# Kernel tuning notes

Hardware: AMD Instinct MI355X
Metric: run time of the kernel (lower is better)

The kernel has to match this reference:

```python
import jax, jax.numpy as jnp
import numpy as np

# Plane-stress elasticity constants (E=1.0, nu=0.3), matching ModelXToResult.__init__
E_MOD = 1.0
NU = 0.3
C11 = E_MOD / (1.0 - NU ** 2)          # = c22
C12 = E_MOD * NU / (1.0 - NU ** 2)     # = c21
C33 = E_MOD / (2.0 * (1.0 + NU))

HIDDEN = 256


def setup_inputs() -> dict:
    key = jax.random.key(0)
    ks = jax.random.split(key, 5)
    B, N = 4, 65536
    X = jax.random.uniform(ks[0], (B, N, 2), dtype=jnp.float32)
    # MLP params (2 -> 256 -> 256 -> 256 -> 2), scaled ~ 1/sqrt(fan_in)
    W1 = jax.random.normal(ks[1], (2, HIDDEN), dtype=jnp.float32) / np.sqrt(2.0)
    b1 = jnp.zeros((HIDDEN,), jnp.float32)
    W2 = jax.random.normal(ks[2], (HIDDEN, HIDDEN), dtype=jnp.float32) / np.sqrt(HIDDEN)
    b2 = jnp.zeros((HIDDEN,), jnp.float32)
    W3 = jax.random.normal(ks[3], (HIDDEN, HIDDEN), dtype=jnp.float32) / np.sqrt(HIDDEN)
    b3 = jnp.zeros((HIDDEN,), jnp.float32)
    Wo = jax.random.normal(ks[4], (HIDDEN, 2), dtype=jnp.float32) / np.sqrt(HIDDEN)
    bo = jnp.zeros((2,), jnp.float32)
    return {"X": X, "W1": W1, "b1": b1, "W2": W2, "b2": b2,
            "W3": W3, "b3": b3, "Wo": Wo, "bo": bo}


def _disp(xy, W1, b1, W2, b2, W3, b3, Wo, bo):
    # xy: [B, N, 2] -> displacement [B, N, 2] = (u, v)
    h = jnp.tanh(xy @ W1 + b1)
    h = jnp.tanh(h @ W2 + b2)
    h = jnp.tanh(h @ W3 + b3)
    return h @ Wo + bo


def reference(X, W1, b1, W2, b2, W3, b3, Wo, bo):
    f = lambda xy: _disp(xy, W1, b1, W2, b2, W3, b3, Wo, bo)
    ones = jnp.ones_like(X[..., 0:1])
    zeros = jnp.zeros_like(ones)
    tx = jnp.concatenate([ones, zeros], axis=-1)  # d/dx tangent
    ty = jnp.concatenate([zeros, ones], axis=-1)  # d/dy tangent
    # Fused forward + full 2x2 Jacobian via two forward-mode JVPs
    out, d_dx = jax.jvp(f, (X,), (tx,))
    _, d_dy = jax.jvp(f, (X,), (ty,))
    u, v = out[..., 0:1], out[..., 1:2]
    u_x, v_x = d_dx[..., 0:1], d_dx[..., 1:2]
    u_y, v_y = d_dy[..., 0:1], d_dy[..., 1:2]
    u_xy = u_y + v_x
    stress_x = C11 * u_x + C12 * v_y
    stress_y = C12 * u_x + C11 * v_y
    stress_xy = C33 * u_xy
    strain_energy_density = 0.5 * (stress_x * u_x + stress_y * v_y + stress_xy * u_xy)
    return (u, v, stress_x, stress_y, stress_xy, strain_energy_density)
```

## Files before the change

### kernel.cpp

```cpp
#include <hip/hip_runtime.h>

#define HIDDEN 256
#define NPTS (4*65536)
#define MTILE 32
#define NWG (NPTS/MTILE)
#define THREADS 512

typedef _Float16 h8  __attribute__((ext_vector_type(8)));
typedef float    f4  __attribute__((ext_vector_type(4)));

__device__ __forceinline__ float tanh_fast(float x){
  float t = exp2f(x * 2.885390081777927f);
  return 1.0f - 2.0f * __builtin_amdgcn_rcpf(t + 1.0f);
}

__device__ __forceinline__ uint2 pack4(float a, float b, float c, float d){
  uint2 r;
  r.x = __builtin_bit_cast(unsigned int, __builtin_amdgcn_cvt_pkrtz(a, b));
  r.y = __builtin_bit_cast(unsigned int, __builtin_amdgcn_cvt_pkrtz(c, d));
  return r;
}

__device__ __forceinline__ int act_off(int p, int ubyte){
  return p*512 + (ubyte ^ ((p & 15) << 4));
}

__global__ void pack_weights(const float* __restrict__ W, _Float16* __restrict__ dst){
  int i = blockIdx.x * blockDim.x + threadIdx.x;
  int l  = i & 63;
  int nt = (i >> 6) & 15;
  int ks = i >> 10;
  int k0 = ks*32 + ((l >> 4) << 3);
  int n  = nt*16 + (l & 15);
  h8 v;
  #pragma unroll
  for (int j = 0; j < 8; ++j) v[j] = (_Float16)W[(k0 + j)*HIDDEN + n];
  *reinterpret_cast<h8*>(dst + (size_t)i*8) = v;
}

__launch_bounds__(THREADS, 4)
__global__ void pinn_fused(const float* __restrict__ X,
                           const float* __restrict__ W1,
                           const float* __restrict__ b1,
                           const float* __restrict__ b2,
                           const float* __restrict__ b3,
                           const float* __restrict__ Wo,
                           const float* __restrict__ bo,
                           const _Float16* __restrict__ Wp,
                           float* __restrict__ out)
{
  __shared__ __align__(16) char actS[3*MTILE*512];

  const int tid = threadIdx.x;
  const int wid = tid >> 6;
  const int l   = tid & 63;
  const int lg  = l >> 4;
  const int lr  = l & 15;
  const int Uq  = wid >> 1;
  const int Pg  = wid & 1;

  {
    const int pl = tid >> 4;
    const int ug = tid & 15;
    const int P  = blockIdx.x * MTILE + pl;
    const float x0 = X[2*P + 0];
    const float x1 = X[2*P + 1];
    #pragma unroll
    for (int c = 0; c < 4; ++c){
      const int u = ug*16 + c*4;
      const f4 w0 = *reinterpret_cast<const f4*>(W1 + u);
      const f4 w1 = *reinterpret_cast<const f4*>(W1 + HIDDEN + u);
      const f4 bb = *reinterpret_cast<const f4*>(b1 + u);
      float h[4], gx[4], gy[4];
      #pragma unroll
      for (int j = 0; j < 4; ++j){
        const float z = x0*w0[j] + x1*w1[j] + bb[j];
        const float t = tanh_fast(z);
        const float s = 1.0f - t*t;
        h[j]  = t;
        gx[j] = s * w0[j];
        gy[j] = s * w1[j];
      }
      const int off = act_off(pl, u*2);
      *reinterpret_cast<uint2*>(actS + 0*16384 + off) = pack4(h[0],h[1],h[2],h[3]);
      *reinterpret_cast<uint2*>(actS + 1*16384 + off) = pack4(gx[0],gx[1],gx[2],gx[3]);
      *reinterpret_cast<uint2*>(actS + 2*16384 + off) = pack4(gy[0],gy[1],gy[2],gy[3]);
    }
  }
  __syncthreads();

  for (int layer = 0; layer < 2; ++layer){
    const _Float16* WL = Wp + layer*65536;
    const float* bl = (layer == 0) ? b2 : b3;

    f4 acc[3][4];
    const f4 fzero = {0.f, 0.f, 0.f, 0.f};
    #pragma unroll
    for (int s = 0; s < 3; ++s)
      #pragma unroll
      for (int ut = 0; ut < 4; ++ut)
        acc[s][ut] = fzero;

    #pragma unroll
    for (int ks = 0; ks < 8; ++ks){
      h8 wf[4];
      #pragma unroll
      for (int ut = 0; ut < 4; ++ut)
        wf[ut] = *reinterpret_cast<const h8*>(WL + ((size_t)((ks*16 + Uq*4 + ut)*64 + l))*8);
      const int p   = Pg*16 + lr;
      const int ub  = ks*64 + lg*16;
      const int off = act_off(p, ub);
      #pragma unroll
      for (int s = 0; s < 3; ++s){
        const h8 af = *reinterpret_cast<const h8*>(actS + s*16384 + off);
        #pragma unroll
        for (int ut = 0; ut < 4; ++ut)
          acc[s][ut] = __builtin_amdgcn_mfma_f32_16x16x32_f16(wf[ut], af, acc[s][ut], 0, 0, 0);
      }
    }
    __syncthreads();

    #pragma unroll
    for (int ut = 0; ut < 4; ++ut){
      const int u0 = Uq*64 + ut*16 + lg*4;
      const f4 bb = *reinterpret_cast<const f4*>(bl + u0);
      const int p  = Pg*16 + lr;
      const f4 z  = acc[0][ut];
      const f4 zx = acc[1][ut];
      const f4 zy = acc[2][ut];
      float h[4], gx[4], gy[4];
      #pragma unroll
      for (int j = 0; j < 4; ++j){
        const float t = tanh_fast(z[j] + bb[j]);
        const float s = 1.0f - t*t;
        h[j]  = t;
        gx[j] = s * zx[j];
        gy[j] = s * zy[j];
      }
      const int off = act_off(p, u0*2);
      *reinterpret_cast<uint2*>(actS + 0*16384 + off) = pack4(h[0],h[1],h[2],h[3]);
      *reinterpret_cast<uint2*>(actS + 1*16384 + off) = pack4(gx[0],gx[1],gx[2],gx[3]);
      *reinterpret_cast<uint2*>(actS + 2*16384 + off) = pack4(gy[0],gy[1],gy[2],gy[3]);
    }
    __syncthreads();
  }

  {
    const int pl = tid >> 4;
    const int kg = tid & 15;
    const int P  = blockIdx.x * MTILE + pl;
    float au=0.f, av=0.f, aux=0.f, avx=0.f, auy=0.f, avy=0.f;
    #pragma unroll
    for (int c = 0; c < 2; ++c){
      const int k0  = kg*16 + c*8;
      const int off = act_off(pl, k0*2);
      const h8 hh = *reinterpret_cast<const h8*>(actS + 0*16384 + off);
      const h8 hx = *reinterpret_cast<const h8*>(actS + 1*16384 + off);
      const h8 hy = *reinterpret_cast<const h8*>(actS + 2*16384 + off);
      #pragma unroll
      for (int j = 0; j < 8; ++j){
        const float2 wo = *reinterpret_cast<const float2*>(Wo + 2*(k0 + j));
        const float fh = (float)hh[j];
        const float fx = (float)hx[j];
        const float fy = (float)hy[j];
        au  += fh*wo.x;  av  += fh*wo.y;
        aux += fx*wo.x;  avx += fx*wo.y;
        auy += fy*wo.x;  avy += fy*wo.y;
      }
    }
    #pragma unroll
    for (int m = 1; m < 16; m <<= 1){
      au  += __shfl_xor(au,  m, 64);
      av  += __shfl_xor(av,  m, 64);
      aux += __shfl_xor(aux, m, 64);
      avx += __shfl_xor(avx, m, 64);
      auy += __shfl_xor(auy, m, 64);
      avy += __shfl_xor(avy, m, 64);
    }
    if (kg == 0){
      const float C11 = 1.0989010989010988f;
      const float C12 = 0.32967032967032966f;
      const float C33 = 0.38461538461538464f;
      const float u  = au + bo[0];
      const float v  = av + bo[1];
      const float ux = aux, vx = avx, uy = auy, vy = avy;
      const float uxy = uy + vx;
      const float sx  = C11*ux + C12*vy;
      const float sy  = C12*ux + C11*vy;
      const float sxy = C33*uxy;
      const float sed = 0.5f*(sx*ux + sy*vy + sxy*uxy);
      out[0*NPTS + P] = u;
      out[1*NPTS + P] = v;
      out[2*NPTS + P] = sx;
      out[3*NPTS + P] = sy;
      out[4*NPTS + P] = sxy;
      out[5*NPTS + P] = sed;
    }
  }
}

extern "C" void kernel_launch(void* const* d_in, const int* in_sizes, int n_in,
                              void* d_out, int out_size, void* d_ws, size_t ws_size,
                              hipStream_t stream)
{
  const float* X  = (const float*)d_in[0];
  const float* W1 = (const float*)d_in[1];
  const float* b1 = (const float*)d_in[2];
  const float* W2 = (const float*)d_in[3];
  const float* b2 = (const float*)d_in[4];
  const float* W3 = (const float*)d_in[5];
  const float* b3 = (const float*)d_in[6];
  const float* Wo = (const float*)d_in[7];
  const float* bo = (const float*)d_in[8];

  _Float16* Wp = (_Float16*)d_ws;

  pack_weights<<<32, 256, 0, stream>>>(W2, Wp);
  pack_weights<<<32, 256, 0, stream>>>(W3, Wp + 65536);
  pinn_fused<<<NWG, THREADS, 0, stream>>>(X, W1, b1, b2, b3, Wo, bo, Wp, (float*)d_out);
}
```

Before: 290.8 us.

## Halve tile to 16 points and fuse output layer into last MFMA epilogue

Shrinks each workgroup to 16 points and 4 waves (256 threads), raising the occupancy hint from 4 to 6, and unrolls the two hidden layers explicitly. The last hidden layer's tanh and its JVP tangents are now reduced directly against Wo in registers instead of being written back to LDS and reread. Partial sums are reduced with cross-lane shuffles and a small LDS buffer shared across waves. This removes one LDS round trip and one barrier per tile. In exchange, each workgroup loads the same packed weights for half as many points, which doubles weight traffic from L2 per point.

```diff
diff --git a/kernel.cpp b/kernel.cpp
--- a/kernel.cpp
+++ b/kernel.cpp
@@ -2,9 +2,9 @@
 
 #define HIDDEN 256
 #define NPTS (4*65536)
-#define MTILE 32
+#define MTILE 16
 #define NWG (NPTS/MTILE)
-#define THREADS 512
+#define THREADS 256
 
 typedef _Float16 h8  __attribute__((ext_vector_type(8)));
 typedef float    f4  __attribute__((ext_vector_type(4)));
@@ -38,7 +38,7 @@
   *reinterpret_cast<h8*>(dst + (size_t)i*8) = v;
 }
 
-__launch_bounds__(THREADS, 4)
+__launch_bounds__(THREADS, 6)
 __global__ void pinn_fused(const float* __restrict__ X,
                            const float* __restrict__ W1,
                            const float* __restrict__ b1,
@@ -50,21 +50,19 @@
                            float* __restrict__ out)
 {
   __shared__ __align__(16) char actS[3*MTILE*512];
+  __shared__ __align__(16) float partS[MTILE*24];
 
   const int tid = threadIdx.x;
-  const int wid = tid >> 6;
   const int l   = tid & 63;
   const int lg  = l >> 4;
   const int lr  = l & 15;
-  const int Uq  = wid >> 1;
-  const int Pg  = wid & 1;
+  const int Uq  = __builtin_amdgcn_readfirstlane(tid >> 6);
 
   {
-    const int pl = tid >> 4;
-    const int ug = tid & 15;
+    const int pl = tid & 15;
+    const int ug = tid >> 4;
     const int P  = blockIdx.x * MTILE + pl;
-    const float x0 = X[2*P + 0];
-    const float x1 = X[2*P + 1];
+    const float2 xy = *reinterpret_cast<const float2*>(X + 2*P);
     #pragma unroll
     for (int c = 0; c < 4; ++c){
       const int u = ug*16 + c*4;
@@ -74,7 +72,7 @@
       float h[4], gx[4], gy[4];
       #pragma unroll
       for (int j = 0; j < 4; ++j){
-        const float z = x0*w0[j] + x1*w1[j] + bb[j];
+        const float z = xy.x*w0[j] + xy.y*w1[j] + bb[j];
         const float t = tanh_fast(z);
         const float s = 1.0f - t*t;
         h[j]  = t;
@@ -82,37 +80,32 @@
         gy[j] = s * w1[j];
       }
       const int off = act_off(pl, u*2);
-      *reinterpret_cast<uint2*>(actS + 0*16384 + off) = pack4(h[0],h[1],h[2],h[3]);
-      *reinterpret_cast<uint2*>(actS + 1*16384 + off) = pack4(gx[0],gx[1],gx[2],gx[3]);
-      *reinterpret_cast<uint2*>(actS + 2*16384 + off) = pack4(gy[0],gy[1],gy[2],gy[3]);
+      *reinterpret_cast<uint2*>(actS + 0*8192 + off) = pack4(h[0],h[1],h[2],h[3]);
+      *reinterpret_cast<uint2*>(actS + 1*8192 + off) = pack4(gx[0],gx[1],gx[2],gx[3]);
+      *reinterpret_cast<uint2*>(actS + 2*8192 + off) = pack4(gy[0],gy[1],gy[2],gy[3]);
     }
   }
   __syncthreads();
 
-  for (int layer = 0; layer < 2; ++layer){
-    const _Float16* WL = Wp + layer*65536;
-    const float* bl = (layer == 0) ? b2 : b3;
-
+  {
+    const _Float16* WL = Wp;
     f4 acc[3][4];
     const f4 fzero = {0.f, 0.f, 0.f, 0.f};
     #pragma unroll
     for (int s = 0; s < 3; ++s)
       #pragma unroll
-      for (int ut = 0; ut < 4; ++ut)
-        acc[s][ut] = fzero;
+      for (int ut = 0; ut < 4; ++ut) acc[s][ut] = fzero;
 
     #pragma unroll
     for (int ks = 0; ks < 8; ++ks){
       h8 wf[4];
       #pragma unroll
       for (int ut = 0; ut < 4; ++ut)
-        wf[ut] = *reinterpret_cast<const h8*>(WL + ((size_t)((ks*16 + Uq*4 + ut)*64 + l))*8);
-      const int p   = Pg*16 + lr;
-      const int ub  = ks*64 + lg*16;
-      const int off = act_off(p, ub);
+        wf[ut] = *reinterpret_cast<const h8*>(WL + (size_t)(((ks*16 + Uq*4 + ut)*64 + l))*8);
+      const int off = act_off(lr, ks*64 + lg*16);
       #pragma unroll
       for (int s = 0; s < 3; ++s){
-        const h8 af = *reinterpret_cast<const h8*>(actS + s*16384 + off);
+        const h8 af = *reinterpret_cast<const h8*>(actS + s*8192 + off);
         #pragma unroll
         for (int ut = 0; ut < 4; ++ut)
           acc[s][ut] = __builtin_amdgcn_mfma_f32_16x16x32_f16(wf[ut], af, acc[s][ut], 0, 0, 0);
@@ -123,8 +116,7 @@
     #pragma unroll
     for (int ut = 0; ut < 4; ++ut){
       const int u0 = Uq*64 + ut*16 + lg*4;
-      const f4 bb = *reinterpret_cast<const f4*>(bl + u0);
-      const int p  = Pg*16 + lr;
+      const f4 bb = *reinterpret_cast<const f4*>(b2 + u0);
       const f4 z  = acc[0][ut];
       const f4 zx = acc[1][ut];
       const f4 zy = acc[2][ut];
@@ -137,39 +129,64 @@
         gx[j] = s * zx[j];
         gy[j] = s * zy[j];
       }
-      const int off = act_off(p, u0*2);
-      *reinterpret_cast<uint2*>(actS + 0*16384 + off) = pack4(h[0],h[1],h[2],h[3]);
-      *reinterpret_cast<uint2*>(actS + 1*16384 + off) = pack4(gx[0],gx[1],gx[2],gx[3]);
-      *reinterpret_cast<uint2*>(actS + 2*16384 + off) = pack4(gy[0],gy[1],gy[2],gy[3]);
+      const int off = act_off(lr, u0*2);
+      *reinterpret_cast<uint2*>(actS + 0*8192 + off) = pack4(h[0],h[1],h[2],h[3]);
+      *reinterpret_cast<uint2*>(actS + 1*8192 + off) = pack4(gx[0],gx[1],gx[2],gx[3]);
+      *reinterpret_cast<uint2*>(actS + 2*8192 + off) = pack4(gy[0],gy[1],gy[2],gy[3]);
     }
     __syncthreads();
   }
 
   {
-    const int pl = tid >> 4;
-    const int kg = tid & 15;
-    const int P  = blockIdx.x * MTILE + pl;
+    const _Float16* WL = Wp + 65536;
+    f4 acc[3][4];
+    const f4 fzero = {0.f, 0.f, 0.f, 0.f};
+    #pragma unroll
+    for (int s = 0; s < 3; ++s)
+      #pragma unroll
+      for (int ut = 0; ut < 4; ++ut) acc[s][ut] = fzero;
+
+    #pragma unroll
+    for (int ks = 0; ks < 8; ++ks){
+      h8 wf[4];
+      #pragma unroll
+      for (int ut = 0; ut < 4; ++ut)
+        wf[ut] = *reinterpret_cast<const h8*>(WL + (size_t)(((ks*16 + Uq*4 + ut)*64 + l))*8);
+      const int off = act_off(lr, ks*64 + lg*16);
+      #pragma unroll
+      for (int s = 0; s < 3; ++s){
+        const h8 af = *reinterpret_cast<const h8*>(actS + s*8192 + off);
+        #pragma unroll
+        for (int ut = 0; ut < 4; ++ut)
+          acc[s][ut] = __builtin_amdgcn_mfma_f32_16x16x32_f16(wf[ut], af, acc[s][ut], 0, 0, 0);
+      }
+    }
+
     float au=0.f, av=0.f, aux=0.f, avx=0.f, auy=0.f, avy=0.f;
     #pragma unroll
-    for (int c = 0; c < 2; ++c){
-      const int k0  = kg*16 + c*8;
-      const int off = act_off(pl, k0*2);
-      const h8 hh = *reinterpret_cast<const h8*>(actS + 0*16384 + off);
-      const h8 hx = *reinterpret_cast<const h8*>(actS + 1*16384 + off);
-      const h8 hy = *reinterpret_cast<const h8*>(actS + 2*16384 + off);
-      #pragma unroll
-      for (int j = 0; j < 8; ++j){
-        const float2 wo = *reinterpret_cast<const float2*>(Wo + 2*(k0 + j));
-        const float fh = (float)hh[j];
-        const float fx = (float)hx[j];
-        const float fy = (float)hy[j];
-        au  += fh*wo.x;  av  += fh*wo.y;
-        aux += fx*wo.x;  avx += fx*wo.y;
-        auy += fy*wo.x;  avy += fy*wo.y;
-      }
-    }
-    #pragma unroll
-    for (int m = 1; m < 16; m <<= 1){
+    for (int ut = 0; ut < 4; ++ut){
+      const int u0 = Uq*64 + ut*16 + lg*4;
+      const f4 bb  = *reinterpret_cast<const f4*>(b3 + u0);
+      const f4 wo0 = *reinterpret_cast<const f4*>(Wo + 2*u0);
+      const f4 wo1 = *reinterpret_cast<const f4*>(Wo + 2*u0 + 4);
+      const f4 z  = acc[0][ut];
+      const f4 zx = acc[1][ut];
+      const f4 zy = acc[2][ut];
+      #pragma unroll
+      for (int j = 0; j < 4; ++j){
+        const float t = tanh_fast(z[j] + bb[j]);
+        const float s = 1.0f - t*t;
+        const float gx = s * zx[j];
+        const float gy = s * zy[j];
+        const float wx = (j < 2) ? wo0[2*(j&1)]   : wo1[2*(j&1)];
+        const float wy = (j < 2) ? wo0[2*(j&1)+1] : wo1[2*(j&1)+1];
+        au  += t*wx;   av  += t*wy;
+        aux += gx*wx;  avx += gx*wy;
+        auy += gy*wx;  avy += gy*wy;
+      }
+    }
+    #pragma unroll
+    for (int m = 16; m <= 32; m <<= 1){
       au  += __shfl_xor(au,  m, 64);
       av  += __shfl_xor(av,  m, 64);
       aux += __shfl_xor(aux, m, 64);
@@ -177,25 +194,43 @@
       auy += __shfl_xor(auy, m, 64);
       avy += __shfl_xor(avy, m, 64);
     }
-    if (kg == 0){
-      const float C11 = 1.0989010989010988f;
-      const float C12 = 0.32967032967032966f;
-      const float C33 = 0.38461538461538464f;
-      const float u  = au + bo[0];
-      const float v  = av + bo[1];
-      const float ux = aux, vx = avx, uy = auy, vy = avy;
-      const float uxy = uy + vx;
-      const float sx  = C11*ux + C12*vy;
-      const float sy  = C12*ux + C11*vy;
-      const float sxy = C33*uxy;
-      const float sed = 0.5f*(sx*ux + sy*vy + sxy*uxy);
-      out[0*NPTS + P] = u;
-      out[1*NPTS + P] = v;
-      out[2*NPTS + P] = sx;
-      out[3*NPTS + P] = sy;
-      out[4*NPTS + P] = sxy;
-      out[5*NPTS + P] = sed;
-    }
+    if (lg == 0){
+      float* pp = partS + lr*24 + Uq*6;
+      *reinterpret_cast<float2*>(pp + 0) = float2{au,  av };
+      *reinterpret_cast<float2*>(pp + 2) = float2{aux, avx};
+      *reinterpret_cast<float2*>(pp + 4) = float2{auy, avy};
+    }
+  }
+  __syncthreads();
+
+  if (tid < MTILE){
+    const int p = tid;
+    const int P = blockIdx.x * MTILE + p;
+    float au=0.f, av=0.f, aux=0.f, avx=0.f, auy=0.f, avy=0.f;
+    #pragma unroll
+    for (int q = 0; q < 4; ++q){
+      const float* pp = partS + p*24 + q*6;
+      const float2 a = *reinterpret_cast<const float2*>(pp + 0);
+      const float2 b = *reinterpret_cast<const float2*>(pp + 2);
+      const float2 c = *reinterpret_cast<const float2*>(pp + 4);
+      au += a.x; av += a.y; aux += b.x; avx += b.y; auy += c.x; avy += c.y;
+    }
+    const float C11 = 1.0989010989010988f;
+    const float C12 = 0.32967032967032966f;
+    const float C33 = 0.38461538461538464f;
+    const float u  = au + bo[0];
+    const float v  = av + bo[1];
+    const float uxy = auy + avx;
+    const float sx  = C11*aux + C12*avy;
+    const float sy  = C12*aux + C11*avy;
+    const float sxy = C33*uxy;
+    const float sed = 0.5f*(sx*aux + sy*avy + sxy*uxy);
+    out[0*NPTS + P] = u;
+    out[1*NPTS + P] = v;
+    out[2*NPTS + P] = sx;
+    out[3*NPTS + P] = sy;
+    out[4*NPTS + P] = sxy;
+    out[5*NPTS + P] = sed;
   }
 }
 
```

After: 592.9 us. 104% more time.
